# Optimization experiments

Measured on AMD Instinct MI355X. Metric: run time of the kernel, lower is better.

The kernel has to match this reference:

```python
import jax, jax.numpy as jnp
import numpy as np

B, S, E, H = 8, 1024, 1024, 16
D = E // H  # head dimension = 64


def setup_inputs() -> dict:
    key = jax.random.key(0)
    ks = jax.random.split(key, 9)
    sc = 1.0 / np.sqrt(E)
    return {
        "q": jax.random.normal(ks[0], (B, S, E), dtype=jnp.float32),
        "Wq_w": jax.random.normal(ks[1], (E, E), dtype=jnp.float32) * sc,
        "Wq_b": jax.random.normal(ks[2], (E,), dtype=jnp.float32) * 0.01,
        "Wk_w": jax.random.normal(ks[3], (E, E), dtype=jnp.float32) * sc,
        "Wk_b": jax.random.normal(ks[4], (E,), dtype=jnp.float32) * 0.01,
        "Wv_w": jax.random.normal(ks[5], (E, E), dtype=jnp.float32) * sc,
        "Wv_b": jax.random.normal(ks[6], (E,), dtype=jnp.float32) * 0.01,
        "Wo_w": jax.random.normal(ks[7], (E, E), dtype=jnp.float32) * sc,
        "Wo_b": jax.random.normal(ks[8], (E,), dtype=jnp.float32) * 0.01,
    }


def reference(q, Wq_w, Wq_b, Wk_w, Wk_b, Wv_w, Wv_b, Wo_w, Wo_b):
    # Linear projections (torch Linear: x @ W.T + b)
    Q = q @ Wq_w.T + Wq_b
    K = q @ Wk_w.T + Wk_b  # self-attention: k = v = q
    V = q @ Wv_w.T + Wv_b
    # [B, S, E] -> [B, H, S, D]
    Q = Q.reshape(B, S, H, D).transpose(0, 2, 1, 3)
    K = K.reshape(B, S, H, D).transpose(0, 2, 1, 3)
    V = V.reshape(B, S, H, D).transpose(0, 2, 1, 3)
    # Scores [B, H, S, S], scaled by sqrt(head_dim)
    scores = jnp.einsum('bhqd,bhkd->bhqk', Q, K) / jnp.sqrt(jnp.float32(D))
    attn = jax.nn.softmax(scores, axis=-1)
    # dropout p=0.0 (eval mode) -> identity
    out = jnp.einsum('bhqk,bhkd->bhqd', attn, V)
    out = out.transpose(0, 2, 1, 3).reshape(B, S, E)
    out = out @ Wo_w.T + Wo_b
    return out, attn
```

## Files before the change

### kernel.cpp

```cpp
#include <hip/hip_runtime.h>

using bf16x8 = __attribute__((ext_vector_type(8))) __bf16;
using f32x4  = __attribute__((ext_vector_type(4))) float;

#define NE 1024
#define C1E 0.18033688011112042f
#define C2E -11.541560327111707f

__device__ __forceinline__ unsigned short f2b(float f) {
    unsigned u = __builtin_bit_cast(unsigned, f);
    u = (u + 0x7FFFu + ((u >> 16) & 1u)) >> 16;
    return (unsigned short)u;
}

typedef __attribute__((address_space(1))) const void gvoid_t;
typedef __attribute__((address_space(3))) void lvoid_t;


__device__ __forceinline__ void stage128(const unsigned short* gbase, char* lds, int tid)
{
    const int w = tid >> 6, l = tid & 63;
    #pragma unroll
    for (int i = 0; i < 4; ++i) {
        int grp = i * 4 + w;
        int row = grp * 8 + (l >> 3);
        int srcb = ((l & 7) * 16) ^ ((l >> 3) << 4);
        const char* g = (const char*)(gbase + (size_t)row * NE) + srcb;
        __builtin_amdgcn_global_load_lds((gvoid_t*)g, (lvoid_t*)(lds + grp * 1024), 16, 0, 0);
    }
}

__device__ __forceinline__ void stage64x128(const unsigned short* gbase, char* lds, int tid)
{
    const int w = tid >> 6, l = tid & 63;
    #pragma unroll
    for (int i = 0; i < 2; ++i) {
        int grp = i * 4 + w;
        int row = grp * 8 + (l >> 3);
        int srcb = ((l & 7) * 16) ^ ((l >> 3) << 4);
        const char* g = (const char*)(gbase + (size_t)row * NE) + srcb;
        __builtin_amdgcn_global_load_lds((gvoid_t*)g, (lvoid_t*)(lds + grp * 1024), 16, 0, 0);
    }
}

__device__ __forceinline__ void stage32(const unsigned short* gbase, char* lds, int tid)
{
    const int w = tid >> 6, l = tid & 63;
    int row = w * 8 + (l >> 3);
    int srcb = ((l & 7) * 16) ^ ((l >> 3) << 4);
    const char* g = (const char*)(gbase + (size_t)row * NE) + srcb;
    __builtin_amdgcn_global_load_lds((gvoid_t*)g, (lvoid_t*)(lds + w * 1024), 16, 0, 0);
}

__device__ __forceinline__ void stage64x256(const unsigned short* gbase, char* lds, int tid)
{
    const int w = tid >> 6, l = tid & 63;
    #pragma unroll
    for (int i = 0; i < 4; ++i) {
        int row0 = i * 16 + w * 4;
        int row = row0 + (l >> 4);
        int srcb = ((l & 15) * 16) ^ ((row & 7) << 4);
        const char* g = (const char*)(gbase + (size_t)row * 1024) + srcb;
        __builtin_amdgcn_global_load_lds((gvoid_t*)g, (lvoid_t*)(lds + row0 * 256), 16, 0, 0);
    }
}

__global__ __launch_bounds__(256)
void conv_bf16(const float* __restrict__ src, unsigned short* __restrict__ dst)
{
    size_t i = ((size_t)blockIdx.x * 256 + threadIdx.x) * 8;
    float4 a0 = *(const float4*)(src + i);
    float4 a1 = *(const float4*)(src + i + 4);
    uint4 p;
    p.x = f2b(a0.x) | ((unsigned)f2b(a0.y) << 16);
    p.y = f2b(a0.z) | ((unsigned)f2b(a0.w) << 16);
    p.z = f2b(a1.x) | ((unsigned)f2b(a1.y) << 16);
    p.w = f2b(a1.z) | ((unsigned)f2b(a1.w) << 16);
    *(uint4*)(dst + i) = p;
}

__global__ __launch_bounds__(256)
void conv_all(const float* __restrict__ q, const float* __restrict__ w0,
              const float* __restrict__ w1, const float* __restrict__ w2,
              unsigned short* __restrict__ qd, unsigned short* __restrict__ d0,
              unsigned short* __restrict__ d1, unsigned short* __restrict__ d2)
{
    int bid = blockIdx.x;
    const float* s; unsigned short* d; size_t off;
    if (bid < 4096) { s = q; d = qd; off = (size_t)bid * 2048; }
    else {
        int seg = (bid - 4096) >> 9, r = (bid - 4096) & 511;
        s = seg == 0 ? w0 : (seg == 1 ? w1 : w2);
        d = seg == 0 ? d0 : (seg == 1 ? d1 : d2);
        off = (size_t)r * 2048;
    }
    size_t i = off + threadIdx.x * 8;
    float4 a0 = *(const float4*)(s + i);
    float4 a1 = *(const float4*)(s + i + 4);
    uint4 p;
    p.x = f2b(a0.x) | ((unsigned)f2b(a0.y) << 16);
    p.y = f2b(a0.z) | ((unsigned)f2b(a0.w) << 16);
    p.z = f2b(a1.x) | ((unsigned)f2b(a1.y) << 16);
    p.w = f2b(a1.z) | ((unsigned)f2b(a1.w) << 16);
    *(uint4*)(d + i) = p;
}

__global__ __launch_bounds__(256, 2)
void qkv_proj(const unsigned short* __restrict__ A,
              const unsigned short* __restrict__ Wq, const unsigned short* __restrict__ Wk,
              const unsigned short* __restrict__ Wv,
              const float* __restrict__ bq, const float* __restrict__ bk,
              const float* __restrict__ bv,
              unsigned short* __restrict__ Qo, unsigned short* __restrict__ Ko,
              unsigned short* __restrict__ Vo)
{
    __shared__ char Asm[16384];
    __shared__ char Bsm[3][8192];
    const int tid  = threadIdx.x;
    const int lane = tid & 63;
    const int w    = tid >> 6;
    const int swz = (blockIdx.x & 7) * 128 + (blockIdx.x >> 3);
    const int rowbase = (swz >> 4) * 128;
    const int colbase = (swz & 15) * 64;
    f32x4 acc[3][2][4] = {};

    for (int kt = 0; kt < 16; ++kt) {
        __syncthreads();
        stage128(A + (size_t)rowbase * NE + kt * 64, Asm, tid);
        stage64x128(Wq + (size_t)colbase * NE + kt * 64, Bsm[0], tid);
        stage64x128(Wk + (size_t)colbase * NE + kt * 64, Bsm[1], tid);
        stage64x128(Wv + (size_t)colbase * NE + kt * 64, Bsm[2], tid);
        __syncthreads();
        #pragma unroll
        for (int ks = 0; ks < 2; ++ks) {
            const int kb = ks * 64 + (lane >> 4) * 16;
            bf16x8 af[2], bf[3][4];
            #pragma unroll
            for (int m = 0; m < 2; ++m) {
                int row = w * 32 + m * 16 + (lane & 15);
                af[m] = *(const bf16x8*)(Asm + ((row * 128 + kb) ^ ((row & 7) << 4)));
            }
            #pragma unroll
            for (int j = 0; j < 3; ++j)
                #pragma unroll
                for (int n = 0; n < 4; ++n) {
                    int row = n * 16 + (lane & 15);
                    bf[j][n] = *(const bf16x8*)(Bsm[j] + ((row * 128 + kb) ^ ((row & 7) << 4)));
                }
            #pragma unroll
            for (int j = 0; j < 3; ++j)
                #pragma unroll
                for (int m = 0; m < 2; ++m)
                    #pragma unroll
                    for (int n = 0; n < 4; ++n)
                        acc[j][m][n] = __builtin_amdgcn_mfma_f32_16x16x32_bf16(af[m], bf[j][n], acc[j][m][n], 0, 0, 0);
        }
    }

    #pragma unroll
    for (int m = 0; m < 2; ++m)
        #pragma unroll
        for (int n = 0; n < 4; ++n) {
            int col = colbase + n * 16 + (lane & 15);
            float bvq = bq[col], bvk = bk[col], bvv = bv[col];
            #pragma unroll
            for (int r = 0; r < 4; ++r) {
                int row = rowbase + w * 32 + m * 16 + (lane >> 4) * 4 + r;
                Qo[(size_t)row * NE + col] = f2b(acc[0][m][n][r] + bvq);
                Ko[(size_t)row * NE + col] = f2b(acc[1][m][n][r] + bvk);
                int b = row >> 10, s = row & 1023, h = col >> 6, d = col & 63;
                Vo[((size_t)((b * 16 + h) * 64 + d) << 10) + s] = f2b(acc[2][m][n][r] + bvv);
            }
        }
}

__global__ __launch_bounds__(256)
void proj_o(const unsigned short* __restrict__ A, const unsigned short* __restrict__ W,
            const float* __restrict__ bias, float* __restrict__ outp)
{
    __shared__ char Asm[16384], Bsm[16384];
    const int tid  = threadIdx.x;
    const int lane = tid & 63;
    const int wid  = tid >> 6;
    const int wr = wid >> 1, wc = wid & 1;
    const int swz = (blockIdx.x & 7) * 64 + (blockIdx.x >> 3);
    const int rowbase = (swz >> 3) * 128;
    const int colbase = (swz & 7) * 128;
    f32x4 acc[4][4] = {};

    for (int kt = 0; kt < 16; ++kt) {
        __syncthreads();
        stage128(A + (size_t)rowbase * NE + kt * 64, Asm, tid);
        stage128(W + (size_t)colbase * NE + kt * 64, Bsm, tid);
        __syncthreads();
        #pragma unroll
        for (int ks = 0; ks < 2; ++ks) {
            const int kb = ks * 64 + (lane >> 4) * 16;
            bf16x8 af[4], bf[4];
            #pragma unroll
            for (int m = 0; m < 4; ++m) {
                int row = wr * 64 + m * 16 + (lane & 15);
                af[m] = *(const bf16x8*)(Asm + ((row * 128 + kb) ^ ((row & 7) << 4)));
            }
            #pragma unroll
            for (int n = 0; n < 4; ++n) {
                int row = wc * 64 + n * 16 + (lane & 15);
                bf[n] = *(const bf16x8*)(Bsm + ((row * 128 + kb) ^ ((row & 7) << 4)));
            }
            #pragma unroll
            for (int m = 0; m < 4; ++m)
                #pragma unroll
                for (int n = 0; n < 4; ++n)
                    acc[m][n] = __builtin_amdgcn_mfma_f32_16x16x32_bf16(af[m], bf[n], acc[m][n], 0, 0, 0);
        }
    }

    #pragma unroll
    for (int m = 0; m < 4; ++m)
        #pragma unroll
        for (int n = 0; n < 4; ++n) {
            int col = colbase + wc * 64 + n * 16 + (lane & 15);
            float bv = bias[col];
            #pragma unroll
            for (int r = 0; r < 4; ++r) {
                int row = rowbase + wr * 64 + m * 16 + (lane >> 4) * 4 + r;
                outp[(size_t)row * NE + col] = acc[m][n][r] + bv;
            }
        }
}

__global__ __launch_bounds__(256, 2)
void fused_attn(const unsigned short* __restrict__ Q,
                const unsigned short* __restrict__ K,
                const unsigned short* __restrict__ VT,
                float* __restrict__ attn, unsigned short* __restrict__ Og)
{
    __shared__ char Ksm[16384];
    __shared__ char Vsm[2][16384];
    __shared__ char Psm[8192];
    __shared__ float rs4[4][32];
    __shared__ float il[32];
    const int tid  = threadIdx.x;
    const int lane = tid & 63;
    const int w    = tid >> 6;
    const int swzb = (blockIdx.x & 7) * 512 + (blockIdx.x >> 3);
    const int bh = swzb >> 5, qt = swzb & 31;
    const int b = bh >> 4, h = bh & 15;
    const unsigned short* Qg = Q  + (size_t)(b * 1024 + qt * 32) * 1024 + h * 64;
    const unsigned short* Kg = K  + (size_t)(b * 1024) * 1024 + h * 64;
    const unsigned short* Vg = VT + (size_t)bh * 64 * 1024;

    stage32(Qg, Psm, tid);
    stage128(Kg, Ksm, tid);
    __syncthreads();
    bf16x8 qf[2][2];
    #pragma unroll
    for (int ks = 0; ks < 2; ++ks) {
        const int kb = ks * 64 + (lane >> 4) * 16;
        #pragma unroll
        for (int n = 0; n < 2; ++n) {
            int row = n * 16 + (lane & 15);
            qf[ks][n] = *(const bf16x8*)(Psm + ((row * 128 + kb) ^ ((row & 7) << 4)));
        }
    }

    f32x4 sacc[8][2][2] = {};
    float rs_p[2] = {0.f, 0.f};
    #pragma unroll
    for (int kt = 0; kt < 8; ++kt) {
        __builtin_amdgcn_s_setprio(1);
        #pragma unroll
        for (int ks = 0; ks < 2; ++ks) {
            const int kb = ks * 64 + (lane >> 4) * 16;
            bf16x8 kf[2];
            #pragma unroll
            for (int m = 0; m < 2; ++m) {
                int row = w * 32 + m * 16 + (lane & 15);
                kf[m] = *(const bf16x8*)(Ksm + ((row * 128 + kb) ^ ((row & 7) << 4)));
            }
            #pragma unroll
            for (int m = 0; m < 2; ++m)
                #pragma unroll
                for (int n = 0; n < 2; ++n)
                    sacc[kt][m][n] = __builtin_amdgcn_mfma_f32_16x16x32_bf16(kf[m], qf[ks][n], sacc[kt][m][n], 0, 0, 0);
        }
        __builtin_amdgcn_s_setprio(0);
        __syncthreads();
        if (kt < 7) stage128(Kg + (size_t)((kt + 1) * 128) * 1024, Ksm, tid);
        else        stage64x256(Vg, Vsm[0], tid);
        #pragma unroll
        for (int m = 0; m < 2; ++m)
            #pragma unroll
            for (int n = 0; n < 2; ++n)
                #pragma unroll
                for (int r = 0; r < 4; ++r) {
                    float e = exp2f(fmaf(sacc[kt][m][n][r], C1E, C2E));
                    sacc[kt][m][n][r] = e;
                    rs_p[n] += e;
                }
        __syncthreads();
    }

    #pragma unroll
    for (int n = 0; n < 2; ++n) {
        rs_p[n] += __shfl_xor(rs_p[n], 16);
        rs_p[n] += __shfl_xor(rs_p[n], 32);
    }
    if (lane < 16) {
        rs4[w][lane]      = rs_p[0];
        rs4[w][16 + lane] = rs_p[1];
    }
    __syncthreads();
    if (tid < 32) il[tid] = 1.0f / (rs4[0][tid] + rs4[1][tid] + rs4[2][tid] + rs4[3][tid]);
    __syncthreads();

    f32x4 oa[2] = {};
    float* attnq = attn + ((size_t)bh * 1024 + qt * 32) * 1024;
    #pragma unroll
    for (int kt = 0; kt < 8; ++kt) {
        #pragma unroll
        for (int n = 0; n < 2; ++n) {
            int q = n * 16 + (lane & 15);
            float iv = il[q];
            #pragma unroll
            for (int m = 0; m < 2; ++m) {
                int k0 = w * 32 + m * 16 + (lane >> 4) * 4;
                float4 p4;
                p4.x = sacc[kt][m][n][0] * iv;
                p4.y = sacc[kt][m][n][1] * iv;
                p4.z = sacc[kt][m][n][2] * iv;
                p4.w = sacc[kt][m][n][3] * iv;
                *(float4*)(attnq + (size_t)q * 1024 + kt * 128 + k0) = p4;
                uint2 pk;
                pk.x = f2b(p4.x) | ((unsigned)f2b(p4.y) << 16);
                pk.y = f2b(p4.z) | ((unsigned)f2b(p4.w) << 16);
                *(uint2*)(Psm + ((q * 256 + k0 * 2) ^ ((q & 7) << 4))) = pk;
            }
        }
        __syncthreads();
        if (kt < 7) stage64x256(Vg + (kt + 1) * 128, Vsm[(kt + 1) & 1], tid);
        __builtin_amdgcn_s_setprio(1);
        #pragma unroll
        for (int ks = 0; ks < 4; ++ks) {
            const int kb = ks * 64 + (lane >> 4) * 16;
            bf16x8 pa[2], vb;
            #pragma unroll
            for (int m2 = 0; m2 < 2; ++m2) {
                int row = m2 * 16 + (lane & 15);
                pa[m2] = *(const bf16x8*)(Psm + ((row * 256 + kb) ^ ((row & 7) << 4)));
            }
            {
                int d = w * 16 + (lane & 15);
                vb = *(const bf16x8*)(Vsm[kt & 1] + d * 256 + (kb ^ ((d & 7) << 4)));
            }
            #pragma unroll
            for (int m2 = 0; m2 < 2; ++m2)
                oa[m2] = __builtin_amdgcn_mfma_f32_16x16x32_bf16(pa[m2], vb, oa[m2], 0, 0, 0);
        }
        __builtin_amdgcn_s_setprio(0);
        __syncthreads();
    }

    unsigned short* Ob = Og + (size_t)(b * 1024 + qt * 32) * 1024 + h * 64;
    #pragma unroll
    for (int m2 = 0; m2 < 2; ++m2) {
        int d = w * 16 + (lane & 15);
        #pragma unroll
        for (int r = 0; r < 4; ++r) {
            int qrow = m2 * 16 + (lane >> 4) * 4 + r;
            Ob[(size_t)qrow * 1024 + d] = f2b(oa[m2][r]);
        }
    }
}

extern "C" void kernel_launch(void* const* d_in, const int* in_sizes, int n_in,
                              void* d_out, int out_size, void* d_ws, size_t ws_size,
                              hipStream_t stream) {
    (void)in_sizes; (void)n_in; (void)out_size; (void)ws_size;
    const float* q    = (const float*)d_in[0];
    const float* Wq_w = (const float*)d_in[1];
    const float* Wq_b = (const float*)d_in[2];
    const float* Wk_w = (const float*)d_in[3];
    const float* Wk_b = (const float*)d_in[4];
    const float* Wv_w = (const float*)d_in[5];
    const float* Wv_b = (const float*)d_in[6];
    const float* Wo_w = (const float*)d_in[7];
    const float* Wo_b = (const float*)d_in[8];

    char* ws = (char*)d_ws;
    unsigned short* Qws  = (unsigned short*)(ws);
    unsigned short* Kws  = (unsigned short*)(ws + (16u << 20));
    unsigned short* VTws = (unsigned short*)(ws + (32u << 20));

    float* outp  = (float*)d_out;
    float* attnp = outp + 8388608;

    char* scr = (char*)attnp;
    unsigned short* qbf = (unsigned short*)scr;
    unsigned short* wqb = (unsigned short*)(scr + (16u << 20));
    unsigned short* wkb = (unsigned short*)(scr + (18u << 20));
    unsigned short* wvb = (unsigned short*)(scr + (20u << 20));

    dim3 blk(256);
    conv_all<<<dim3(4096 + 3 * 512), blk, 0, stream>>>(q, Wq_w, Wk_w, Wv_w, qbf, wqb, wkb, wvb);
    qkv_proj<<<dim3(1024), blk, 0, stream>>>(qbf, wqb, wkb, wvb, Wq_b, Wk_b, Wv_b, Qws, Kws, VTws);
    fused_attn<<<dim3(4096), blk, 0, stream>>>(Qws, Kws, VTws, attnp, Qws);
    conv_bf16<<<dim3(512), blk, 0, stream>>>(Wo_w, Kws);
    proj_o<<<dim3(512), blk, 0, stream>>>(Qws, Kws, Wo_b, outp);
}
```

Baseline: 344.2 us.

## Use 128-query tiles with two-pass score recompute instead of caching scores in registers

The attention kernel now processes 128 query rows per block instead of 32, cutting the grid from 4096 to 1024 blocks and reusing each staged K/V tile across four times as many queries. Scores are no longer held in registers across the whole key range. A first pass computes row sums of exp, a second pass recomputes QK^T and applies exp with a folded log-normalizer, then does the PV product. This cuts K/V global traffic per query, but it doubles the QK^T MFMA and exp work. It also drops V double buffering and lowers occupancy because of larger LDS use and more registers.

```diff
diff --git a/kernel.cpp b/kernel.cpp
--- a/kernel.cpp
+++ b/kernel.cpp
@@ -41,15 +41,6 @@
         const char* g = (const char*)(gbase + (size_t)row * NE) + srcb;
         __builtin_amdgcn_global_load_lds((gvoid_t*)g, (lvoid_t*)(lds + grp * 1024), 16, 0, 0);
     }
-}
-
-__device__ __forceinline__ void stage32(const unsigned short* gbase, char* lds, int tid)
-{
-    const int w = tid >> 6, l = tid & 63;
-    int row = w * 8 + (l >> 3);
-    int srcb = ((l & 7) * 16) ^ ((l >> 3) << 4);
-    const char* g = (const char*)(gbase + (size_t)row * NE) + srcb;
-    __builtin_amdgcn_global_load_lds((gvoid_t*)g, (lvoid_t*)(lds + w * 1024), 16, 0, 0);
 }
 
 __device__ __forceinline__ void stage64x256(const unsigned short* gbase, char* lds, int tid)
@@ -236,38 +227,38 @@
                 float* __restrict__ attn, unsigned short* __restrict__ Og)
 {
     __shared__ char Ksm[16384];
-    __shared__ char Vsm[2][16384];
-    __shared__ char Psm[8192];
-    __shared__ float rs4[4][32];
-    __shared__ float il[32];
+    __shared__ char Vsm[16384];
+    __shared__ char Psm[32768];
+    __shared__ float rs4[4][128];
+    __shared__ float lt[128];
     const int tid  = threadIdx.x;
     const int lane = tid & 63;
     const int w    = tid >> 6;
-    const int swzb = (blockIdx.x & 7) * 512 + (blockIdx.x >> 3);
-    const int bh = swzb >> 5, qt = swzb & 31;
+    const int swzb = (blockIdx.x & 7) * 128 + (blockIdx.x >> 3);
+    const int bh = swzb >> 3, qt = swzb & 7;
     const int b = bh >> 4, h = bh & 15;
-    const unsigned short* Qg = Q  + (size_t)(b * 1024 + qt * 32) * 1024 + h * 64;
+    const unsigned short* Qg = Q  + (size_t)(b * 1024 + qt * 128) * 1024 + h * 64;
     const unsigned short* Kg = K  + (size_t)(b * 1024) * 1024 + h * 64;
     const unsigned short* Vg = VT + (size_t)bh * 64 * 1024;
 
-    stage32(Qg, Psm, tid);
-    stage128(Kg, Ksm, tid);
+    stage128(Qg, Psm, tid);
     __syncthreads();
-    bf16x8 qf[2][2];
+    bf16x8 qf[2][8];
     #pragma unroll
     for (int ks = 0; ks < 2; ++ks) {
         const int kb = ks * 64 + (lane >> 4) * 16;
         #pragma unroll
-        for (int n = 0; n < 2; ++n) {
+        for (int n = 0; n < 8; ++n) {
             int row = n * 16 + (lane & 15);
             qf[ks][n] = *(const bf16x8*)(Psm + ((row * 128 + kb) ^ ((row & 7) << 4)));
         }
     }
-
-    f32x4 sacc[8][2][2] = {};
-    float rs_p[2] = {0.f, 0.f};
-    #pragma unroll
+    stage128(Kg, Ksm, tid);
+
+    float rs_p[8] = {0.f, 0.f, 0.f, 0.f, 0.f, 0.f, 0.f, 0.f};
     for (int kt = 0; kt < 8; ++kt) {
+        __syncthreads();
+        f32x4 sa[2][8] = {};
         __builtin_amdgcn_s_setprio(1);
         #pragma unroll
         for (int ks = 0; ks < 2; ++ks) {
@@ -281,55 +272,71 @@
             #pragma unroll
             for (int m = 0; m < 2; ++m)
                 #pragma unroll
-                for (int n = 0; n < 2; ++n)
-                    sacc[kt][m][n] = __builtin_amdgcn_mfma_f32_16x16x32_bf16(kf[m], qf[ks][n], sacc[kt][m][n], 0, 0, 0);
+                for (int n = 0; n < 8; ++n)
+                    sa[m][n] = __builtin_amdgcn_mfma_f32_16x16x32_bf16(kf[m], qf[ks][n], sa[m][n], 0, 0, 0);
         }
         __builtin_amdgcn_s_setprio(0);
         __syncthreads();
         if (kt < 7) stage128(Kg + (size_t)((kt + 1) * 128) * 1024, Ksm, tid);
-        else        stage64x256(Vg, Vsm[0], tid);
-        #pragma unroll
-        for (int m = 0; m < 2; ++m)
-            #pragma unroll
-            for (int n = 0; n < 2; ++n)
-                #pragma unroll
-                for (int r = 0; r < 4; ++r) {
-                    float e = exp2f(fmaf(sacc[kt][m][n][r], C1E, C2E));
-                    sacc[kt][m][n][r] = e;
-                    rs_p[n] += e;
-                }
-        __syncthreads();
-    }
-
-    #pragma unroll
-    for (int n = 0; n < 2; ++n) {
+        #pragma unroll
+        for (int n = 0; n < 8; ++n)
+            #pragma unroll
+            for (int m = 0; m < 2; ++m)
+                #pragma unroll
+                for (int r = 0; r < 4; ++r)
+                    rs_p[n] += exp2f(fmaf(sa[m][n][r], C1E, C2E));
+    }
+    #pragma unroll
+    for (int n = 0; n < 8; ++n) {
         rs_p[n] += __shfl_xor(rs_p[n], 16);
         rs_p[n] += __shfl_xor(rs_p[n], 32);
     }
     if (lane < 16) {
-        rs4[w][lane]      = rs_p[0];
-        rs4[w][16 + lane] = rs_p[1];
+        #pragma unroll
+        for (int n = 0; n < 8; ++n) rs4[w][n * 16 + lane] = rs_p[n];
     }
     __syncthreads();
-    if (tid < 32) il[tid] = 1.0f / (rs4[0][tid] + rs4[1][tid] + rs4[2][tid] + rs4[3][tid]);
-    __syncthreads();
-
-    f32x4 oa[2] = {};
-    float* attnq = attn + ((size_t)bh * 1024 + qt * 32) * 1024;
-    #pragma unroll
+    if (tid < 128) {
+        float l = rs4[0][tid] + rs4[1][tid] + rs4[2][tid] + rs4[3][tid];
+        lt[tid] = C2E - __log2f(l);
+    }
+    stage128(Kg, Ksm, tid);
+
+    f32x4 oa[2][4] = {};
+    float* attnq = attn + ((size_t)bh * 1024 + qt * 128) * 1024;
     for (int kt = 0; kt < 8; ++kt) {
-        #pragma unroll
-        for (int n = 0; n < 2; ++n) {
+        __syncthreads();
+        stage64x256(Vg + kt * 128, Vsm, tid);
+        f32x4 sa[2][8] = {};
+        __builtin_amdgcn_s_setprio(1);
+        #pragma unroll
+        for (int ks = 0; ks < 2; ++ks) {
+            const int kb = ks * 64 + (lane >> 4) * 16;
+            bf16x8 kf[2];
+            #pragma unroll
+            for (int m = 0; m < 2; ++m) {
+                int row = w * 32 + m * 16 + (lane & 15);
+                kf[m] = *(const bf16x8*)(Ksm + ((row * 128 + kb) ^ ((row & 7) << 4)));
+            }
+            #pragma unroll
+            for (int m = 0; m < 2; ++m)
+                #pragma unroll
+                for (int n = 0; n < 8; ++n)
+                    sa[m][n] = __builtin_amdgcn_mfma_f32_16x16x32_bf16(kf[m], qf[ks][n], sa[m][n], 0, 0, 0);
+        }
+        __builtin_amdgcn_s_setprio(0);
+        #pragma unroll
+        for (int n = 0; n < 8; ++n) {
             int q = n * 16 + (lane & 15);
-            float iv = il[q];
+            float ltq = lt[q];
             #pragma unroll
             for (int m = 0; m < 2; ++m) {
                 int k0 = w * 32 + m * 16 + (lane >> 4) * 4;
                 float4 p4;
-                p4.x = sacc[kt][m][n][0] * iv;
-                p4.y = sacc[kt][m][n][1] * iv;
-                p4.z = sacc[kt][m][n][2] * iv;
-                p4.w = sacc[kt][m][n][3] * iv;
+                p4.x = exp2f(fmaf(sa[m][n][0], C1E, ltq));
+                p4.y = exp2f(fmaf(sa[m][n][1], C1E, ltq));
+                p4.z = exp2f(fmaf(sa[m][n][2], C1E, ltq));
+                p4.w = exp2f(fmaf(sa[m][n][3], C1E, ltq));
                 *(float4*)(attnq + (size_t)q * 1024 + kt * 128 + k0) = p4;
                 uint2 pk;
                 pk.x = f2b(p4.x) | ((unsigned)f2b(p4.y) << 16);
@@ -338,39 +345,42 @@
             }
         }
         __syncthreads();
-        if (kt < 7) stage64x256(Vg + (kt + 1) * 128, Vsm[(kt + 1) & 1], tid);
+        if (kt < 7) stage128(Kg + (size_t)((kt + 1) * 128) * 1024, Ksm, tid);
         __builtin_amdgcn_s_setprio(1);
         #pragma unroll
         for (int ks = 0; ks < 4; ++ks) {
             const int kb = ks * 64 + (lane >> 4) * 16;
-            bf16x8 pa[2], vb;
+            bf16x8 pa[2], vb[4];
             #pragma unroll
             for (int m2 = 0; m2 < 2; ++m2) {
-                int row = m2 * 16 + (lane & 15);
+                int row = w * 32 + m2 * 16 + (lane & 15);
                 pa[m2] = *(const bf16x8*)(Psm + ((row * 256 + kb) ^ ((row & 7) << 4)));
             }
-            {
-                int d = w * 16 + (lane & 15);
-                vb = *(const bf16x8*)(Vsm[kt & 1] + d * 256 + (kb ^ ((d & 7) << 4)));
+            #pragma unroll
+            for (int n2 = 0; n2 < 4; ++n2) {
+                int d = n2 * 16 + (lane & 15);
+                vb[n2] = *(const bf16x8*)(Vsm + d * 256 + (kb ^ ((d & 7) << 4)));
             }
             #pragma unroll
             for (int m2 = 0; m2 < 2; ++m2)
-                oa[m2] = __builtin_amdgcn_mfma_f32_16x16x32_bf16(pa[m2], vb, oa[m2], 0, 0, 0);
+                #pragma unroll
+                for (int n2 = 0; n2 < 4; ++n2)
+                    oa[m2][n2] = __builtin_amdgcn_mfma_f32_16x16x32_bf16(pa[m2], vb[n2], oa[m2][n2], 0, 0, 0);
         }
         __builtin_amdgcn_s_setprio(0);
-        __syncthreads();
-    }
-
-    unsigned short* Ob = Og + (size_t)(b * 1024 + qt * 32) * 1024 + h * 64;
-    #pragma unroll
-    for (int m2 = 0; m2 < 2; ++m2) {
-        int d = w * 16 + (lane & 15);
-        #pragma unroll
-        for (int r = 0; r < 4; ++r) {
-            int qrow = m2 * 16 + (lane >> 4) * 4 + r;
-            Ob[(size_t)qrow * 1024 + d] = f2b(oa[m2][r]);
-        }
-    }
+    }
+    unsigned short* Ob = Og + (size_t)(b * 1024 + qt * 128) * 1024 + h * 64;
+    #pragma unroll
+    for (int m2 = 0; m2 < 2; ++m2)
+        #pragma unroll
+        for (int n2 = 0; n2 < 4; ++n2) {
+            int d = n2 * 16 + (lane & 15);
+            #pragma unroll
+            for (int r = 0; r < 4; ++r) {
+                int qrow = w * 32 + m2 * 16 + (lane >> 4) * 4 + r;
+                Ob[(size_t)qrow * 1024 + d] = f2b(oa[m2][n2][r]);
+            }
+        }
 }
 
 extern "C" void kernel_launch(void* const* d_in, const int* in_sizes, int n_in,
@@ -404,7 +414,7 @@
     dim3 blk(256);
     conv_all<<<dim3(4096 + 3 * 512), blk, 0, stream>>>(q, Wq_w, Wk_w, Wv_w, qbf, wqb, wkb, wvb);
     qkv_proj<<<dim3(1024), blk, 0, stream>>>(qbf, wqb, wkb, wvb, Wq_b, Wk_b, Wv_b, Qws, Kws, VTws);
-    fused_attn<<<dim3(4096), blk, 0, stream>>>(Qws, Kws, VTws, attnp, Qws);
+    fused_attn<<<dim3(1024), blk, 0, stream>>>(Qws, Kws, VTws, attnp, Qws);
     conv_bf16<<<dim3(512), blk, 0, stream>>>(Wo_w, Kws);
     proj_o<<<dim3(512), blk, 0, stream>>>(Qws, Kws, Wo_b, outp);
 }
```

Result: faster. 278.0 us (-19.2%).
